# Kernel optimization log

Hardware: AMD Instinct MI355X
Metric: run time of the kernel (lower is better)

## Reference

```python
import jax, jax.numpy as jnp
import numpy as np

IMAGE_SIZE = 256
PSIZE = 6
STRIDE = 2
WINDOW = IMAGE_SIZE + 1 - PSIZE  # 251
CUR = np.arange(0, WINDOW, STRIDE)
if CUR[-1] != WINDOW - 1:
    CUR = np.concatenate([CUR, np.array([WINDOW - 1])])
NPOS = len(CUR)  # 126 strided window positions per axis
BATCH = 128


def setup_inputs() -> dict:
    key = jax.random.key(0)
    x = jax.random.normal(key, (BATCH, 1, IMAGE_SIZE, IMAGE_SIZE), dtype=jnp.float32)
    return {"x": x}


def reference(x):
    # Equivalent to patch_tf.forward(to_patch): for each strided window position
    # (r, c) in CUR x CUR and each in-patch offset (i, j) in [0, PSIZE)^2,
    # output[b, r*NPOS + c, i*PSIZE + j] = x[b, 0, r + i, c + j].
    cur = jnp.asarray(CUR, dtype=jnp.int32)          # [NPOS]
    off = jnp.arange(PSIZE, dtype=jnp.int32)         # [PSIZE]
    row_idx = cur[:, None] + off[None, :]            # [NPOS, PSIZE]
    col_idx = cur[:, None] + off[None, :]            # [NPOS, PSIZE]
    img = x[:, 0]                                    # [B, H, W]
    # Advanced-index gather -> [B, NPOS, NPOS, PSIZE, PSIZE]
    patches = img[:, row_idx[:, None, :, None], col_idx[None, :, None, :]]
    return patches.reshape(x.shape[0], NPOS * NPOS, PSIZE * PSIZE)
```

## Files before the change

kernel.cpp:

```cpp
#include <hip/hip_runtime.h>


#define IMG 256
#define PSZ 6
#define NPOS 126
#define BATCHN 128
#define LDSW 267
#define NV 1134
#define NXCD 8

__global__ __launch_bounds__(256) void image2patch_kernel(
    const float* __restrict__ x, float* __restrict__ out) {
  __shared__ float tile[PSZ * LDSW];

  const int cpx = (BATCHN * NPOS) / NXCD;
  const int raw = blockIdx.x;
  const int blk = (raw % NXCD) * cpx + raw / NXCD;

  const int b = blk / NPOS;
  const int i = blk - b * NPOS;
  const int t = threadIdx.x;

  const float* src = x + (size_t)b * (IMG * IMG) + (size_t)(2 * i) * IMG;
  for (int idx = t; idx < PSZ * (IMG / 4); idx += 256) {
    const int col4 = idx / PSZ;
    const int row  = idx - col4 * PSZ;
    float4 v = reinterpret_cast<const float4*>(src + row * IMG)[col4];
    float* d = &tile[row * LDSW + col4 * 4];
    d[0] = v.x; d[1] = v.y; d[2] = v.z; d[3] = v.w;
  }
  __syncthreads();

  if (t < 252) {
    const int tj = t / 9;
    const int m  = t - 9 * tj;
    const int k0 = 4 * m;
    int a0, a1, a2, a3;
    {
      const int k = k0;     const int r = k / PSZ, c = k - PSZ * r; a0 = r * LDSW + 2 * tj + c;
    }
    {
      const int k = k0 + 1; const int r = k / PSZ, c = k - PSZ * r; a1 = r * LDSW + 2 * tj + c;
    }
    {
      const int k = k0 + 2; const int r = k / PSZ, c = k - PSZ * r; a2 = r * LDSW + 2 * tj + c;
    }
    {
      const int k = k0 + 3; const int r = k / PSZ, c = k - PSZ * r; a3 = r * LDSW + 2 * tj + c;
    }
    float4* outp = reinterpret_cast<float4*>(
        out + ((size_t)b * (NPOS * NPOS) + (size_t)i * NPOS) * (PSZ * PSZ));
    int q = t;
#pragma unroll
    for (int it = 0; it < 4; ++it) {
      float4 v;
      v.x = tile[a0]; v.y = tile[a1]; v.z = tile[a2]; v.w = tile[a3];
      outp[q] = v;
      a0 += 56; a1 += 56; a2 += 56; a3 += 56;
      q += 252;
    }
    if (t < 126) {
      float4 v;
      v.x = tile[a0]; v.y = tile[a1]; v.z = tile[a2]; v.w = tile[a3];
      outp[q] = v;
    }
  }
}

extern "C" void kernel_launch(void* const* d_in, const int* in_sizes, int n_in,
                              void* d_out, int out_size, void* d_ws, size_t ws_size,
                              hipStream_t stream) {
  const float* x = (const float*)d_in[0];
  float* out = (float*)d_out;
  image2patch_kernel<<<BATCHN * NPOS, 256, 0, stream>>>(x, out);
}
```

Before: 313.3 us.

## Process nine patch rows per block with an 8-row LDS ring buffer and prefetch

Each block now covers nine consecutive window rows of one image instead of one. An 8-row LDS ring buffer keeps the overlapping rows, so each new window row needs only two fresh image rows, which are prefetched into registers while the current row's patches are written out. The aim is to cut redundant global reads (6 rows per output row down to about 2) and per-block launch overhead. In exchange the grid shrinks to 1792 blocks, and each block executes sequential iterations with a barrier per tile, which lowers parallelism on a write-bound kernel.

```diff
diff --git a/kernel.cpp b/kernel.cpp
--- a/kernel.cpp
+++ b/kernel.cpp
@@ -6,64 +6,87 @@
 #define NPOS 126
 #define BATCHN 128
 #define LDSW 267
-#define NV 1134
+#define TILES 9
+#define NIB (NPOS / TILES)
+#define NBLK (BATCHN * NIB)
 #define NXCD 8
 
 __global__ __launch_bounds__(256) void image2patch_kernel(
     const float* __restrict__ x, float* __restrict__ out) {
-  __shared__ float tile[PSZ * LDSW];
+  __shared__ float ring[8 * LDSW];
 
-  const int cpx = (BATCHN * NPOS) / NXCD;
+  const int cpx = NBLK / NXCD;
   const int raw = blockIdx.x;
   const int blk = (raw % NXCD) * cpx + raw / NXCD;
 
-  const int b = blk / NPOS;
-  const int i = blk - b * NPOS;
-  const int t = threadIdx.x;
+  const int b  = blk / NIB;
+  const int i0 = (blk - b * NIB) * TILES;
+  const int t  = threadIdx.x;
 
-  const float* src = x + (size_t)b * (IMG * IMG) + (size_t)(2 * i) * IMG;
+  const float* img = x + (size_t)b * (IMG * IMG);
+
   for (int idx = t; idx < PSZ * (IMG / 4); idx += 256) {
     const int col4 = idx / PSZ;
-    const int row  = idx - col4 * PSZ;
-    float4 v = reinterpret_cast<const float4*>(src + row * IMG)[col4];
-    float* d = &tile[row * LDSW + col4 * 4];
+    const int rr   = idx - col4 * PSZ;
+    const int R    = 2 * i0 + rr;
+    float4 v = reinterpret_cast<const float4*>(img + (size_t)R * IMG)[col4];
+    float* d = &ring[(R & 7) * LDSW + col4 * 4];
     d[0] = v.x; d[1] = v.y; d[2] = v.z; d[3] = v.w;
   }
+
+  const int tj = t / 9;
+  const int m  = t - 9 * tj;
+  const int k0 = 4 * m;
+  const int kA = k0,     rA = kA / PSZ, cA = 2 * tj + (kA - PSZ * rA);
+  const int kB = k0 + 1, rB = kB / PSZ, cB = 2 * tj + (kB - PSZ * rB);
+  const int kC = k0 + 2, rC = kC / PSZ, cC = 2 * tj + (kC - PSZ * rC);
+  const int kD = k0 + 3, rD = kD / PSZ, cD = 2 * tj + (kD - PSZ * rD);
+
+  const int pr  = t & 1;
+  const int pc4 = t >> 1;
+
   __syncthreads();
 
-  if (t < 252) {
-    const int tj = t / 9;
-    const int m  = t - 9 * tj;
-    const int k0 = 4 * m;
-    int a0, a1, a2, a3;
-    {
-      const int k = k0;     const int r = k / PSZ, c = k - PSZ * r; a0 = r * LDSW + 2 * tj + c;
+  for (int tt = 0; tt < TILES; ++tt) {
+    const int i   = i0 + tt;
+    const int R2i = 2 * i;
+
+    float4 pf;
+    const bool do_pf = (t < 128) && (tt < TILES - 1);
+    if (do_pf) {
+      const int R = R2i + 6 + pr;
+      pf = reinterpret_cast<const float4*>(img + (size_t)R * IMG)[pc4];
     }
-    {
-      const int k = k0 + 1; const int r = k / PSZ, c = k - PSZ * r; a1 = r * LDSW + 2 * tj + c;
+
+    if (t < 252) {
+      int a0 = ((R2i + rA) & 7) * LDSW + cA;
+      int a1 = ((R2i + rB) & 7) * LDSW + cB;
+      int a2 = ((R2i + rC) & 7) * LDSW + cC;
+      int a3 = ((R2i + rD) & 7) * LDSW + cD;
+      float4* outp = reinterpret_cast<float4*>(
+          out + ((size_t)b * (NPOS * NPOS) + (size_t)i * NPOS) * (PSZ * PSZ));
+      int q = t;
+#pragma unroll
+      for (int it = 0; it < 4; ++it) {
+        float4 v;
+        v.x = ring[a0]; v.y = ring[a1]; v.z = ring[a2]; v.w = ring[a3];
+        outp[q] = v;
+        a0 += 56; a1 += 56; a2 += 56; a3 += 56;
+        q += 252;
+      }
+      if (t < 126) {
+        float4 v;
+        v.x = ring[a0]; v.y = ring[a1]; v.z = ring[a2]; v.w = ring[a3];
+        outp[q] = v;
+      }
     }
-    {
-      const int k = k0 + 2; const int r = k / PSZ, c = k - PSZ * r; a2 = r * LDSW + 2 * tj + c;
+
+    if (do_pf) {
+      const int R = R2i + 6 + pr;
+      float* d = &ring[(R & 7) * LDSW + pc4 * 4];
+      d[0] = pf.x; d[1] = pf.y; d[2] = pf.z; d[3] = pf.w;
     }
-    {
-      const int k = k0 + 3; const int r = k / PSZ, c = k - PSZ * r; a3 = r * LDSW + 2 * tj + c;
-    }
-    float4* outp = reinterpret_cast<float4*>(
-        out + ((size_t)b * (NPOS * NPOS) + (size_t)i * NPOS) * (PSZ * PSZ));
-    int q = t;
-#pragma unroll
-    for (int it = 0; it < 4; ++it) {
-      float4 v;
-      v.x = tile[a0]; v.y = tile[a1]; v.z = tile[a2]; v.w = tile[a3];
-      outp[q] = v;
-      a0 += 56; a1 += 56; a2 += 56; a3 += 56;
-      q += 252;
-    }
-    if (t < 126) {
-      float4 v;
-      v.x = tile[a0]; v.y = tile[a1]; v.z = tile[a2]; v.w = tile[a3];
-      outp[q] = v;
-    }
+    __syncthreads();
   }
 }
 
@@ -72,5 +95,5 @@
                               hipStream_t stream) {
   const float* x = (const float*)d_in[0];
   float* out = (float*)d_out;
-  image2patch_kernel<<<BATCHN * NPOS, 256, 0, stream>>>(x, out);
+  image2patch_kernel<<<NBLK, 256, 0, stream>>>(x, out);
 }
```

Result: slower. 326.8 us (+4.3%).
